# Kernel optimization log

Measured on AMD Instinct MI355X. Metric: run time of the kernel, lower is better.

Reference implementation:

```python
import jax, jax.numpy as jnp
import numpy as np

B, N, D = 8, 8192, 512
WS = 128          # ATTENTION_WINDOW_SIZE
LB = 1            # ATTENTION_WINDOW_LOOKBACK (look_backward)
NW = N // WS      # number of windows (N divisible by WS -> autopad no-op)


def setup_inputs() -> dict:
    key = jax.random.key(0)
    ks = jax.random.split(key, 4)
    s = 0.02
    return {
        "x": jax.random.normal(ks[0], (B, N, D), dtype=jnp.float32),
        "w_q": jax.random.normal(ks[1], (D, D), dtype=jnp.float32) * s,
        "b_q": jnp.zeros((D,), dtype=jnp.float32),
        "w_k": jax.random.normal(ks[2], (D, D), dtype=jnp.float32) * s,
        "b_k": jnp.zeros((D,), dtype=jnp.float32),
        "w_v": jax.random.normal(ks[3], (D, D), dtype=jnp.float32) * s,
        "b_v": jnp.zeros((D,), dtype=jnp.float32),
    }


def _look_around(t, pad_value):
    # t: (B, NW, WS, ...) -> concat of [backward..current] windows along window-length axis
    pad_width = [(0, 0), (LB, 0)] + [(0, 0)] * (t.ndim - 2)
    padded = jnp.pad(t, pad_width, constant_values=pad_value)
    return jnp.concatenate([padded[:, i:i + NW] for i in range(LB + 1)], axis=2)


def _local_attention(q, k, v):
    scale = D ** -0.5
    bq = q.reshape(B, NW, WS, D)
    bk = _look_around(k.reshape(B, NW, WS, D), 0.0)   # (B, NW, (LB+1)*WS, D)
    bv = _look_around(v.reshape(B, NW, WS, D), 0.0)

    # absolute position ticks for causal + padding masks
    tq = jnp.arange(N).reshape(1, NW, WS)                               # query positions
    tk = _look_around(jnp.arange(N).reshape(1, NW, WS), -1)             # key positions, -1 = pad

    sim = jnp.einsum('bwie,bwje->bwij', bq, bk) * scale                 # (B, NW, WS, (LB+1)*WS)
    mask = (tq[..., :, None] < tk[..., None, :]) | (tk[..., None, :] < 0)
    sim = jnp.where(mask, -jnp.finfo(sim.dtype).max, sim)
    attn = jax.nn.softmax(sim, axis=-1)                                  # dropout = 0 -> no-op
    out = jnp.einsum('bwij,bwje->bwie', attn, bv)
    return out.reshape(B, N, D)


def reference(x, w_q, b_q, w_k, b_k, w_v, b_v):
    q = x @ w_q.T + b_q
    k = x @ w_k.T + b_k
    v = x @ w_v.T + b_v
    return _local_attention(q, k, v)
```

## Files before the change

kernel.cpp:

```cpp
#include <hip/hip_runtime.h>


typedef __bf16 bf16x8 __attribute__((ext_vector_type(8)));
typedef float f32x4 __attribute__((ext_vector_type(4)));
typedef unsigned short u16x8 __attribute__((ext_vector_type(8)));

#define BATCH 8
#define SEQ   8192
#define DIM   512
#define NWIN  64
#define TOKS  (BATCH * SEQ)
#define WSELEM ((size_t)TOKS * DIM)

__device__ __forceinline__ unsigned short f2b(float f) {
    union { float f; unsigned int u; } c; c.f = f;
    unsigned int u = c.u;
    return (unsigned short)((u + 0x7FFFu + ((u >> 16) & 1u)) >> 16);
}

__device__ __forceinline__ int swz64(int row, int col) {
    return (row * 64 + col) ^ ((row & 7) << 3);
}

__device__ __forceinline__ void gload_lds16(const unsigned short* g,
                                            unsigned short* l) {
    __builtin_amdgcn_global_load_lds(
        (const __attribute__((address_space(1))) void*)g,
        (__attribute__((address_space(3))) void*)l, 16, 0, 0);
}

#define VMCNT(n) asm volatile("s_waitcnt vmcnt(" #n ")" ::: "memory")

__global__ __launch_bounds__(256) void k_cvt(const float* __restrict__ s,
                                             unsigned short* __restrict__ d,
                                             int n8) {
    const int stride = gridDim.x * blockDim.x;
    for (int i = blockIdx.x * blockDim.x + threadIdx.x; i < n8; i += stride) {
        const float4 a = ((const float4*)s)[2 * i];
        const float4 b = ((const float4*)s)[2 * i + 1];
        u16x8 v;
        v[0] = f2b(a.x); v[1] = f2b(a.y); v[2] = f2b(a.z); v[3] = f2b(a.w);
        v[4] = f2b(b.x); v[5] = f2b(b.y); v[6] = f2b(b.z); v[7] = f2b(b.w);
        ((u16x8*)d)[i] = v;
    }
}

__global__ __launch_bounds__(512, 2) void k_qkv(
    const unsigned short* __restrict__ xb, const unsigned short* __restrict__ wb,
    const float* __restrict__ bq, const float* __restrict__ bk,
    const float* __restrict__ bv,
    unsigned short* __restrict__ qo, unsigned short* __restrict__ ko,
    unsigned short* __restrict__ vto)
{
    __shared__ __align__(16) unsigned short sm[73728];
    int bid = (int)blockIdx.x;
    bid = (bid & 7) * 384 + (bid >> 3);
    const int mt = bid / 6, nt = bid - mt * 6;
    const int rbase = mt << 7;
    const int op  = nt >> 1;
    const int cop = (nt & 1) << 8;

    const unsigned short* __restrict__ xsrc0 = xb + ((size_t)rbase << 9);
    const unsigned short* __restrict__ bsrc0 = wb + ((size_t)nt << 17);

    const int tid  = threadIdx.x;
    const int lane = tid & 63;
    const int wid  = tid >> 6;
    const int wm = wid >> 2, wn = wid & 3;
    const int l15 = lane & 15, lg = lane >> 4;

    f32x4 acc[4][4];
#pragma unroll
    for (int m = 0; m < 4; ++m)
#pragma unroll
        for (int n = 0; n < 4; ++n) acc[m][n] = (f32x4){0.f, 0.f, 0.f, 0.f};

    const int r0 = tid >> 3;
    const int sl = tid & 7;

    auto stage = [&](int t) {
        unsigned short* buf = sm + (t % 3) * 24576;
        const int kc = t << 6;
#pragma unroll
        for (int i = 0; i < 2; ++i) {
            const int r = (i << 6) + r0;
            gload_lds16(xsrc0 + ((size_t)r << 9) + kc + ((sl ^ (r & 7)) << 3),
                        buf + (i << 12) + (tid << 3));
        }
#pragma unroll
        for (int i = 0; i < 4; ++i) {
            const int r = (i << 6) + r0;
            gload_lds16(bsrc0 + ((size_t)r << 9) + kc + ((sl ^ (r & 7)) << 3),
                        buf + 8192 + (i << 12) + (tid << 3));
        }
    };

    stage(0);
    stage(1);
    VMCNT(6);
    __builtin_amdgcn_s_barrier();

#pragma unroll
    for (int t = 0; t < 8; ++t) {
        if (t < 6) stage(t + 2);
        const unsigned short* Ab = sm + (t % 3) * 24576;
        const unsigned short* Bb = Ab + 8192;
#pragma unroll
        for (int kk = 0; kk < 2; ++kk) {
            const int cu = (kk << 5) + (lg << 3);
            bf16x8 af[4], bfr[4];
#pragma unroll
            for (int m = 0; m < 4; ++m)
                af[m] = *(const bf16x8*)&Ab[swz64((wm << 6) + (m << 4) + l15, cu)];
#pragma unroll
            for (int n = 0; n < 4; ++n)
                bfr[n] = *(const bf16x8*)&Bb[swz64((wn << 6) + (n << 4) + l15, cu)];
#pragma unroll
            for (int m = 0; m < 4; ++m)
#pragma unroll
                for (int n = 0; n < 4; ++n)
                    acc[m][n] = __builtin_amdgcn_mfma_f32_16x16x32_bf16(
                        af[m], bfr[n], acc[m][n], 0, 0, 0);
        }
        if (t < 6) { VMCNT(6); }
        else if (t == 6) { VMCNT(0); }
        if (t < 7) __builtin_amdgcn_s_barrier();
    }

    if (op < 2) {
        unsigned short* __restrict__ out = op ? ko : qo;
        const float* __restrict__ bias = op ? bk : bq;
#pragma unroll
        for (int n = 0; n < 4; ++n) {
            const int col = cop + (wn << 6) + (n << 4) + l15;
            const float bv_ = bias[col];
#pragma unroll
            for (int m = 0; m < 4; ++m)
#pragma unroll
                for (int j = 0; j < 4; ++j) {
                    const int row = rbase + (wm << 6) + (m << 4) + (lg << 2) + j;
                    out[(size_t)row * DIM + col] = f2b(acc[m][n][j] + bv_);
                }
        }
    } else {
        __syncthreads();
#pragma unroll
        for (int n = 0; n < 4; ++n) {
            const int dvl = (wn << 6) + (n << 4) + l15;
            const float bv_ = bv[cop + dvl];
#pragma unroll
            for (int m = 0; m < 4; ++m)
#pragma unroll
                for (int j = 0; j < 4; ++j) {
                    const int tok = (wm << 6) + (m << 4) + (lg << 2) + j;
                    sm[tok * 264 + dvl] = f2b(acc[m][n][j] + bv_);
                }
        }
        __syncthreads();
        const int batch = rbase >> 13;
        const int c5_0  = (rbase & 8191) >> 5;
        const int keyo  = (tid & 3) << 3;
#pragma unroll
        for (int s = 0; s < 8; ++s) {
            const int c5sel = s & 3, h = s >> 2;
            const int dvl  = (h << 7) + (tid >> 2);
            const int tok0 = (c5sel << 5) + keyo;
            u16x8 v;
#pragma unroll
            for (int j = 0; j < 8; ++j) v[j] = sm[(tok0 + j) * 264 + dvl];
            *(u16x8*)&vto[((size_t)((batch * 256 + c5_0 + c5sel) * 512
                                    + cop + dvl) << 5) + keyo] = v;
        }
    }
}

__global__ __launch_bounds__(512, 2) void k_attn(
    const unsigned short* __restrict__ q,
    const unsigned short* __restrict__ k,
    const unsigned short* __restrict__ vt3,
    float* __restrict__ out)
{
    __shared__ __align__(16) unsigned short Kb[32768];
    __shared__ __align__(16) unsigned short Pl[32768];

    int bid = (int)blockIdx.x;
    bid = (bid & 7) * 64 + (bid >> 3);
    const int b = bid >> 6, w = bid & 63;
    const int tid  = threadIdx.x;
    const int lane = tid & 63, wid = tid >> 6;
    const int l15 = lane & 15, lg = lane >> 4;
    const int kstart = (w - 1) << 7;
    const size_t qrow0 = ((size_t)b << 13) + ((size_t)w << 7);
    const size_t kbase = (size_t)b << 13;

    const int srow = tid >> 3;
    const int s0   = tid & 7;

    f32x4 acc[16];
#pragma unroll
    for (int n = 0; n < 16; ++n) acc[n] = (f32x4){0.f, 0.f, 0.f, 0.f};

    auto stageK = [&](int buf, int ds) {
#pragma unroll
        for (int i = 0; i < 4; ++i) {
            const int r = (i << 6) + srow;
            int krow = kstart + r; krow = krow < 0 ? 0 : krow;
            gload_lds16(k + (kbase + krow) * DIM + (ds << 6) + ((s0 ^ (r & 7)) << 3),
                        Kb + (buf << 14) + (i << 12) + (tid << 3));
        }
    };

    stageK(0, 0);
    stageK(1, 1);
    __syncthreads();
    for (int ds = 0; ds < 8; ++ds) {
        const unsigned short* Kc = Kb + ((ds & 1) << 14);
#pragma unroll
        for (int kk2 = 0; kk2 < 2; ++kk2) {
            const int cu = (kk2 << 5) + (lg << 3);
            const bf16x8 af = *(const bf16x8*)
                &q[(qrow0 + (wid << 4) + l15) * DIM + (ds << 6) + cu];
#pragma unroll
            for (int n = 0; n < 16; ++n) {
                const bf16x8 bf = *(const bf16x8*)&Kc[swz64((n << 4) + l15, cu)];
                acc[n] = __builtin_amdgcn_mfma_f32_16x16x32_bf16(af, bf, acc[n], 0, 0, 0);
            }
        }
        __syncthreads();
        if (ds + 2 < 8) stageK(ds & 1, ds + 2);
    }

    const int c5base = kstart >> 5;
    auto stageV = [&](int buf, int kk) {
        int c5 = c5base + kk; c5 = c5 < 0 ? 0 : c5;
        const unsigned short* src = vt3 + ((size_t)(b * 256 + c5) << 14);
#pragma unroll
        for (int i = 0; i < 4; ++i)
            gload_lds16(src + (i << 12) + (tid << 3),
                        Kb + (buf << 14) + (i << 12) + (tid << 3));
    };
    stageV(0, 0);
    stageV(1, 1);

    const float scale = 0.04419417382415922f;
    float inv[4];
    unsigned short* Pw = Pl + (wid << 12);
#pragma unroll
    for (int jj = 0; jj < 4; ++jj) {
        const int r  = (lg << 2) + jj;
        const int qr = (wid << 4) + r;
        float mx = -3.0e38f;
#pragma unroll
        for (int n = 0; n < 16; ++n) {
            const int c = (n << 4) + l15;
            const bool keep = (c <= qr + 128) && (w > 0 || c >= 128);
            const float s = keep ? acc[n][jj] * scale : -INFINITY;
            acc[n][jj] = s;
            mx = fmaxf(mx, s);
        }
#pragma unroll
        for (int o = 1; o < 16; o <<= 1) mx = fmaxf(mx, __shfl_xor(mx, o));
        float sum = 0.f;
#pragma unroll
        for (int n = 0; n < 16; ++n) {
            const float p = __expf(acc[n][jj] - mx);
            acc[n][jj] = p;
            sum += p;
        }
#pragma unroll
        for (int o = 1; o < 16; o <<= 1) sum += __shfl_xor(sum, o);
        inv[jj] = 1.0f / sum;
#pragma unroll
        for (int n = 0; n < 16; ++n) {
            const int c = (n << 4) + l15;
            Pw[(r << 8) + ((((c >> 3) ^ r) << 3) | (c & 7))] = f2b(acc[n][jj]);
        }
    }
    __syncthreads();

    f32x4 oacc[32];
#pragma unroll
    for (int n = 0; n < 32; ++n) oacc[n] = (f32x4){0.f, 0.f, 0.f, 0.f};

    for (int kk = 0; kk < 8; ++kk) {
        const unsigned short* Vc = Kb + ((kk & 1) << 14);
        const bf16x8 pa = *(const bf16x8*)
            &Pw[(l15 << 8) + ((((kk << 2) + lg) ^ l15) << 3)];
#pragma unroll
        for (int n = 0; n < 32; ++n) {
            const bf16x8 bv_ = *(const bf16x8*)&Vc[(((n << 4) + l15) << 5) + (lg << 3)];
            oacc[n] = __builtin_amdgcn_mfma_f32_16x16x32_bf16(pa, bv_, oacc[n], 0, 0, 0);
        }
        if (kk < 7) {
            __syncthreads();
            if (kk + 2 < 8) stageV(kk & 1, kk + 2);
        }
    }

#pragma unroll
    for (int n = 0; n < 32; ++n) {
        const int dv = (n << 4) + l15;
        float* orow = out + (qrow0 + (wid << 4) + (lg << 2)) * DIM + dv;
#pragma unroll
        for (int jj = 0; jj < 4; ++jj)
            orow[(size_t)jj * DIM] = oacc[n][jj] * inv[jj];
    }
}

extern "C" void kernel_launch(void* const* d_in, const int* in_sizes, int n_in,
                              void* d_out, int out_size, void* d_ws, size_t ws_size,
                              hipStream_t stream) {
    (void)in_sizes; (void)n_in; (void)out_size; (void)ws_size;
    const float* x  = (const float*)d_in[0];
    const float* wq = (const float*)d_in[1];
    const float* bq = (const float*)d_in[2];
    const float* wk = (const float*)d_in[3];
    const float* bk = (const float*)d_in[4];
    const float* wv = (const float*)d_in[5];
    const float* bv = (const float*)d_in[6];
    float* out = (float*)d_out;

    unsigned short* qws  = (unsigned short*)d_ws;
    unsigned short* kws  = qws + WSELEM;
    unsigned short* vtws = kws + WSELEM;

    unsigned short* xbuf = (unsigned short*)d_out;
    unsigned short* wbuf = xbuf + WSELEM;

    k_cvt<<<2048, 256, 0, stream>>>(x, xbuf, (int)(WSELEM / 8));
    k_cvt<<<128, 256, 0, stream>>>(wq, wbuf, DIM * DIM / 8);
    k_cvt<<<128, 256, 0, stream>>>(wk, wbuf + DIM * DIM, DIM * DIM / 8);
    k_cvt<<<128, 256, 0, stream>>>(wv, wbuf + 2 * DIM * DIM, DIM * DIM / 8);
    k_qkv<<<3072, 512, 0, stream>>>(xbuf, wbuf, bq, bk, bv, qws, kws, vtws);
    k_attn<<<512, 512, 0, stream>>>(qws, kws, vtws, out);
}
```

Before: 260.2 us.

## Enlarge QKV GEMM tile to 256 rows with four-stage K-32 pipeline

New measurement: 268.7 us. 3.3% more time.

```diff
diff --git a/kernel.cpp b/kernel.cpp
--- a/kernel.cpp
+++ b/kernel.cpp
@@ -22,14 +22,18 @@
     return (row * 64 + col) ^ ((row & 7) << 3);
 }
 
+__device__ __forceinline__ int swzp(int row, int cu) {
+    const int p = row >> 1;
+    const int q = (((row & 1) << 2) | (cu >> 3)) ^ (p & 7);
+    return p * 64 + q * 8;
+}
+
 __device__ __forceinline__ void gload_lds16(const unsigned short* g,
                                             unsigned short* l) {
     __builtin_amdgcn_global_load_lds(
         (const __attribute__((address_space(1))) void*)g,
         (__attribute__((address_space(3))) void*)l, 16, 0, 0);
 }
-
-#define VMCNT(n) asm volatile("s_waitcnt vmcnt(" #n ")" ::: "memory")
 
 __global__ __launch_bounds__(256) void k_cvt(const float* __restrict__ s,
                                              unsigned short* __restrict__ d,
@@ -52,124 +56,150 @@
     unsigned short* __restrict__ qo, unsigned short* __restrict__ ko,
     unsigned short* __restrict__ vto)
 {
-    __shared__ __align__(16) unsigned short sm[73728];
+    __shared__ __align__(16) unsigned short sm[65536];
+
     int bid = (int)blockIdx.x;
-    bid = (bid & 7) * 384 + (bid >> 3);
-    const int mt = bid / 6, nt = bid - mt * 6;
-    const int rbase = mt << 7;
-    const int op  = nt >> 1;
-    const int cop = (nt & 1) << 8;
+    bid = (bid & 7) * 192 + (bid >> 3);
+    const int mt = bid / 6, ntile = bid - mt * 6;
+    const int rbase = mt << 8;
+    const int op  = ntile >> 1;
+    const int cop = (ntile & 1) << 8;
 
     const unsigned short* __restrict__ xsrc0 = xb + ((size_t)rbase << 9);
-    const unsigned short* __restrict__ bsrc0 = wb + ((size_t)nt << 17);
+    const unsigned short* __restrict__ bsrc0 = wb + ((size_t)ntile << 17);
 
     const int tid  = threadIdx.x;
     const int lane = tid & 63;
     const int wid  = tid >> 6;
     const int wm = wid >> 2, wn = wid & 3;
     const int l15 = lane & 15, lg = lane >> 4;
-
-    f32x4 acc[4][4];
-#pragma unroll
-    for (int m = 0; m < 4; ++m)
+    const int cu = lg << 3;
+
+    f32x4 acc[8][4];
+#pragma unroll
+    for (int m = 0; m < 8; ++m)
 #pragma unroll
         for (int n = 0; n < 4; ++n) acc[m][n] = (f32x4){0.f, 0.f, 0.f, 0.f};
 
-    const int r0 = tid >> 3;
-    const int sl = tid & 7;
-
-    auto stage = [&](int t) {
-        unsigned short* buf = sm + (t % 3) * 24576;
-        const int kc = t << 6;
-#pragma unroll
-        for (int i = 0; i < 2; ++i) {
-            const int r = (i << 6) + r0;
-            gload_lds16(xsrc0 + ((size_t)r << 9) + kc + ((sl ^ (r & 7)) << 3),
-                        buf + (i << 12) + (tid << 3));
-        }
-#pragma unroll
-        for (int i = 0; i < 4; ++i) {
-            const int r = (i << 6) + r0;
-            gload_lds16(bsrc0 + ((size_t)r << 9) + kc + ((sl ^ (r & 7)) << 3),
-                        buf + 8192 + (i << 12) + (tid << 3));
-        }
+    int srow[2], scol[2];
+#pragma unroll
+    for (int i = 0; i < 2; ++i) {
+        const int s = (i << 9) + tid;
+        const int p = s >> 3;
+        const int e = (s & 7) ^ (p & 7);
+        srow[i] = (p << 1) + (e >> 2);
+        scol[i] = (e & 3) << 3;
+    }
+
+    auto stageA = [&](int t) {
+        unsigned short* dst = sm + ((t & 3) << 14);
+        const int kc = t << 5;
+#pragma unroll
+        for (int i = 0; i < 2; ++i)
+            gload_lds16(xsrc0 + ((size_t)srow[i] << 9) + kc + scol[i],
+                        dst + (((i << 9) + tid) << 3));
     };
-
-    stage(0);
-    stage(1);
-    VMCNT(6);
+    auto stageB = [&](int t) {
+        unsigned short* dst = sm + ((t & 3) << 14) + 8192;
+        const int kc = t << 5;
+#pragma unroll
+        for (int i = 0; i < 2; ++i)
+            gload_lds16(bsrc0 + ((size_t)srow[i] << 9) + kc + scol[i],
+                        dst + (((i << 9) + tid) << 3));
+    };
+
+    stageA(0); stageB(0); stageA(1); stageB(1);
+    asm volatile("s_waitcnt vmcnt(4)" ::: "memory");
     __builtin_amdgcn_s_barrier();
 
-#pragma unroll
-    for (int t = 0; t < 8; ++t) {
-        if (t < 6) stage(t + 2);
-        const unsigned short* Ab = sm + (t % 3) * 24576;
-        const unsigned short* Bb = Ab + 8192;
-#pragma unroll
-        for (int kk = 0; kk < 2; ++kk) {
-            const int cu = (kk << 5) + (lg << 3);
-            bf16x8 af[4], bfr[4];
-#pragma unroll
-            for (int m = 0; m < 4; ++m)
-                af[m] = *(const bf16x8*)&Ab[swz64((wm << 6) + (m << 4) + l15, cu)];
-#pragma unroll
-            for (int n = 0; n < 4; ++n)
-                bfr[n] = *(const bf16x8*)&Bb[swz64((wn << 6) + (n << 4) + l15, cu)];
-#pragma unroll
-            for (int m = 0; m < 4; ++m)
-#pragma unroll
-                for (int n = 0; n < 4; ++n)
-                    acc[m][n] = __builtin_amdgcn_mfma_f32_16x16x32_bf16(
-                        af[m], bfr[n], acc[m][n], 0, 0, 0);
-        }
-        if (t < 6) { VMCNT(6); }
-        else if (t == 6) { VMCNT(0); }
-        if (t < 7) __builtin_amdgcn_s_barrier();
+    for (int t = 0; t < 16; ++t) {
+        const unsigned short* Ap = sm + ((t & 3) << 14);
+        const unsigned short* Bp = Ap + 8192;
+        bf16x8 af[4], bf[4];
+#pragma unroll
+        for (int mf = 0; mf < 4; ++mf)
+            af[mf] = *(const bf16x8*)&Ap[swzp((wm << 7) + (mf << 4) + l15, cu)];
+#pragma unroll
+        for (int nf = 0; nf < 4; ++nf)
+            bf[nf] = *(const bf16x8*)&Bp[swzp((wn << 6) + (nf << 4) + l15, cu)];
+        if (t < 14) stageA(t + 2);
+        __builtin_amdgcn_s_barrier();
+        __builtin_amdgcn_s_setprio(1);
+#pragma unroll
+        for (int mf = 0; mf < 4; ++mf)
+#pragma unroll
+            for (int nf = 0; nf < 4; ++nf)
+                acc[mf][nf] = __builtin_amdgcn_mfma_f32_16x16x32_bf16(
+                    af[mf], bf[nf], acc[mf][nf], 0, 0, 0);
+        __builtin_amdgcn_s_setprio(0);
+        __builtin_amdgcn_s_barrier();
+        bf16x8 ag[4];
+#pragma unroll
+        for (int mf = 0; mf < 4; ++mf)
+            ag[mf] = *(const bf16x8*)&Ap[swzp((wm << 7) + ((mf + 4) << 4) + l15, cu)];
+        if (t < 14) stageB(t + 2);
+        __builtin_amdgcn_s_barrier();
+        __builtin_amdgcn_s_setprio(1);
+#pragma unroll
+        for (int mf = 0; mf < 4; ++mf)
+#pragma unroll
+            for (int nf = 0; nf < 4; ++nf)
+                acc[mf + 4][nf] = __builtin_amdgcn_mfma_f32_16x16x32_bf16(
+                    ag[mf], bf[nf], acc[mf + 4][nf], 0, 0, 0);
+        __builtin_amdgcn_s_setprio(0);
+        if (t < 14)       asm volatile("s_waitcnt vmcnt(4)" ::: "memory");
+        else if (t == 14) asm volatile("s_waitcnt vmcnt(0)" ::: "memory");
+        __builtin_amdgcn_s_barrier();
     }
 
     if (op < 2) {
         unsigned short* __restrict__ out = op ? ko : qo;
         const float* __restrict__ bias = op ? bk : bq;
 #pragma unroll
-        for (int n = 0; n < 4; ++n) {
-            const int col = cop + (wn << 6) + (n << 4) + l15;
+        for (int nf = 0; nf < 4; ++nf) {
+            const int col = cop + (wn << 6) + (nf << 4) + l15;
             const float bv_ = bias[col];
 #pragma unroll
-            for (int m = 0; m < 4; ++m)
+            for (int mf = 0; mf < 8; ++mf)
 #pragma unroll
                 for (int j = 0; j < 4; ++j) {
-                    const int row = rbase + (wm << 6) + (m << 4) + (lg << 2) + j;
-                    out[(size_t)row * DIM + col] = f2b(acc[m][n][j] + bv_);
+                    const int row = rbase + (wm << 7) + (mf << 4) + (lg << 2) + j;
+                    out[(size_t)row * DIM + col] = f2b(acc[mf][nf][j] + bv_);
                 }
         }
     } else {
-        __syncthreads();
-#pragma unroll
-        for (int n = 0; n < 4; ++n) {
-            const int dvl = (wn << 6) + (n << 4) + l15;
-            const float bv_ = bv[cop + dvl];
-#pragma unroll
-            for (int m = 0; m < 4; ++m)
-#pragma unroll
-                for (int j = 0; j < 4; ++j) {
-                    const int tok = (wm << 6) + (m << 4) + (lg << 2) + j;
-                    sm[tok * 264 + dvl] = f2b(acc[m][n][j] + bv_);
+        const int batch = rbase >> 13;
+        const int keyo  = (tid & 3) << 3;
+#pragma unroll
+        for (int h = 0; h < 2; ++h) {
+            if (wm == h) {
+#pragma unroll
+                for (int nf = 0; nf < 4; ++nf) {
+                    const int dvl = (wn << 6) + (nf << 4) + l15;
+                    const float bv_ = bv[cop + dvl];
+#pragma unroll
+                    for (int mf = 0; mf < 8; ++mf)
+#pragma unroll
+                        for (int j = 0; j < 4; ++j) {
+                            const int tok = (mf << 4) + (lg << 2) + j;
+                            sm[tok * 264 + dvl] = f2b(acc[mf][nf][j] + bv_);
+                        }
                 }
-        }
-        __syncthreads();
-        const int batch = rbase >> 13;
-        const int c5_0  = (rbase & 8191) >> 5;
-        const int keyo  = (tid & 3) << 3;
-#pragma unroll
-        for (int s = 0; s < 8; ++s) {
-            const int c5sel = s & 3, h = s >> 2;
-            const int dvl  = (h << 7) + (tid >> 2);
-            const int tok0 = (c5sel << 5) + keyo;
-            u16x8 v;
-#pragma unroll
-            for (int j = 0; j < 8; ++j) v[j] = sm[(tok0 + j) * 264 + dvl];
-            *(u16x8*)&vto[((size_t)((batch * 256 + c5_0 + c5sel) * 512
-                                    + cop + dvl) << 5) + keyo] = v;
+            }
+            __syncthreads();
+            const int c5_0 = (((rbase & 8191) + (h << 7)) >> 5);
+#pragma unroll
+            for (int s = 0; s < 8; ++s) {
+                const int c5sel = s & 3, hv = s >> 2;
+                const int dvl  = (hv << 7) + (tid >> 2);
+                const int tok0 = (c5sel << 5) + keyo;
+                u16x8 v;
+#pragma unroll
+                for (int j = 0; j < 8; ++j) v[j] = sm[(tok0 + j) * 264 + dvl];
+                *(u16x8*)&vto[((size_t)((batch * 256 + c5_0 + c5sel) * 512
+                                        + cop + dvl) << 5) + keyo] = v;
+            }
+            __syncthreads();
         }
     }
 }
@@ -331,6 +361,6 @@
     k_cvt<<<128, 256, 0, stream>>>(wq, wbuf, DIM * DIM / 8);
     k_cvt<<<128, 256, 0, stream>>>(wk, wbuf + DIM * DIM, DIM * DIM / 8);
     k_cvt<<<128, 256, 0, stream>>>(wv, wbuf + 2 * DIM * DIM, DIM * DIM / 8);
-    k_qkv<<<3072, 512, 0, stream>>>(xbuf, wbuf, bq, bk, bv, qws, kws, vtws);
+    k_qkv<<<1536, 512, 0, stream>>>(xbuf, wbuf, bq, bk, bv, qws, kws, vtws);
     k_attn<<<512, 512, 0, stream>>>(qws, kws, vtws, out);
 }
```
